# Kernel optimization log

Measured on AMD Instinct MI355X. Metric: run time of the kernel, lower is better.

Reference implementation:

```python
import jax, jax.numpy as jnp
import numpy as np


def setup_inputs() -> dict:
    key = jax.random.key(0)
    k1, k2, k3, k4 = jax.random.split(key, 4)
    B, N, M, D = 8, 2048, 2048, 256
    x = jax.random.normal(k1, (B, N, D), dtype=jnp.float32)
    Fi = jax.random.normal(k2, (B, M, D), dtype=jnp.float32)
    # nn.Linear(dim, dim) params (W applied as x @ W.T + b); scale like torch default
    bound = 1.0 / np.sqrt(D)
    W = jax.random.uniform(k3, (D, D), dtype=jnp.float32, minval=-bound, maxval=bound)
    b = jax.random.uniform(k4, (D,), dtype=jnp.float32, minval=-bound, maxval=bound)
    return {"x": x, "Fi": Fi, "W": W, "b": b}


def reference(x, Fi, W, b):
    # x: [B, N, D], Fi: [B, M, D]
    q = jnp.einsum("bnd,ed->bne", x, W) + b          # linear projection
    scores = jnp.einsum("bnd,bmd->bnm", q, Fi)        # QK^T (no scaling in original)
    attn = jax.nn.softmax(scores, axis=-1)            # softmax over keys
    out = jnp.einsum("bnm,bmd->bnd", attn, Fi)        # attention @ V (V = Fi)
    return out
```

## Files before the change

### kernel.cpp

```cpp
#include <hip/hip_runtime.h>
#include <hip/hip_bf16.h>

typedef _Float16 half8 __attribute__((ext_vector_type(8)));
typedef float floatx4 __attribute__((ext_vector_type(4)));

#define MFMA16H(a, b, c) __builtin_amdgcn_mfma_f32_16x16x32_f16((a), (b), (c), 0, 0, 0)

static constexpr int Bb = 8, Nn = 2048, Mm = 2048, Dd = 256;
static constexpr int FT_ROWS = 272;

__device__ inline void async16(const void* g, void* l)
{
    __builtin_amdgcn_global_load_lds((const __attribute__((address_space(1))) unsigned int*)g,
                                     (__attribute__((address_space(3))) unsigned int*)l,
                                     16, 0, 0);
}

__device__ inline half8 cvt8h(const float* __restrict__ p)
{
    float4 f0 = *reinterpret_cast<const float4*>(p);
    float4 f1 = *reinterpret_cast<const float4*>(p + 4);
    half8 r;
    r[0] = (_Float16)f0.x; r[1] = (_Float16)f0.y; r[2] = (_Float16)f0.z; r[3] = (_Float16)f0.w;
    r[4] = (_Float16)f1.x; r[5] = (_Float16)f1.y; r[6] = (_Float16)f1.z; r[7] = (_Float16)f1.w;
    return r;
}

__device__ inline void cvt8h_split(const float* __restrict__ p, half8& h, half8& l)
{
    float4 f0 = *reinterpret_cast<const float4*>(p);
    float4 f1 = *reinterpret_cast<const float4*>(p + 4);
    float f[8] = {f0.x, f0.y, f0.z, f0.w, f1.x, f1.y, f1.z, f1.w};
#pragma unroll
    for (int i = 0; i < 8; ++i) {
        _Float16 hh = (_Float16)f[i];
        h[i] = hh;
        l[i] = (_Float16)(f[i] - (float)hh);
    }
}

__global__ __launch_bounds__(256, 4)
void prep_kernel(const float* __restrict__ Fi, const float* __restrict__ W,
                 _Float16* __restrict__ FiH, _Float16* __restrict__ FiT,
                 _Float16* __restrict__ Wh, _Float16* __restrict__ Wl)
{
    const int bid = blockIdx.x;
    const int t = threadIdx.x;

    if (bid >= 1056) {
        const int idx = (bid - 1056) * 256 + t;
        const long e = (long)idx * 16;
        const int b  = (int)(e >> 15);
        const int rem = (int)(e & 32767);
        const int rr = rem >> 11;
        const int key = rem & 2047;
        _Float16 v = (rr == 0) ? (_Float16)1.0f : (_Float16)0.0f;
        union { half8 h; uint4 u; } pk;
#pragma unroll
        for (int i = 0; i < 8; ++i) pk.h[i] = v;
        unsigned short* dst = reinterpret_cast<unsigned short*>(FiT)
            + ((size_t)b * FT_ROWS + 256 + rr) * Mm + key;
        *(uint4*)dst       = pk.u;
        *(uint4*)(dst + 8) = pk.u;
        return;
    }
    if (bid >= 1024) {
        const size_t base = (size_t)(bid - 1024) * 2048 + t * 8;
        half8 h, l;
        cvt8h_split(W + base, h, l);
        *(half8*)(Wh + base) = h;
        *(half8*)(Wl + base) = l;
        return;
    }

    __shared__ __align__(16) unsigned short tile[64][72];
    const int b  = bid >> 7;
    const int mt = (bid >> 2) & 31;
    const int dt = bid & 3;
    {
        const int i = t >> 2, jc = (t & 3) * 16;
        const float* src = Fi + ((size_t)b * Mm + mt * 64 + i) * Dd + dt * 64 + jc;
        union { half8 v; uint4 u; } p0, p1;
        p0.v = cvt8h(src);
        p1.v = cvt8h(src + 8);
        *(uint4*)&tile[i][jc]     = p0.u;
        *(uint4*)&tile[i][jc + 8] = p1.u;
        unsigned short* dh = reinterpret_cast<unsigned short*>(FiH)
            + ((size_t)b * Mm + mt * 64 + i) * Dd + dt * 64 + jc;
        *(uint4*)dh       = p0.u;
        *(uint4*)(dh + 8) = p1.u;
    }
    __syncthreads();
    {
        const int d = t >> 2, mc = (t & 3) * 16;
        unsigned short* dst = reinterpret_cast<unsigned short*>(FiT)
            + ((size_t)b * FT_ROWS + dt * 64 + d) * Mm + mt * 64 + mc;
        union { uint4 v[2]; unsigned short s[16]; } u;
#pragma unroll
        for (int s = 0; s < 16; ++s) u.s[s] = tile[mc + s][d];
        *(uint4*)dst       = u.v[0];
        *(uint4*)(dst + 8) = u.v[1];
    }
}

__global__ __launch_bounds__(128, 2)
void qproj_kernel(const float* __restrict__ x, const _Float16* __restrict__ Wh,
                  const _Float16* __restrict__ Wl, const float* __restrict__ bias,
                  _Float16* __restrict__ q)
{
    const int lane = threadIdx.x & 63;
    const int w = threadIdx.x >> 6;
    const int lo = lane & 15, hi = lane >> 4;
    const long r0 = (long)blockIdx.x * 32;

    floatx4 acc[2][8];
#pragma unroll
    for (int rt = 0; rt < 2; ++rt)
#pragma unroll
        for (int j = 0; j < 8; ++j) acc[rt][j] = (floatx4)0.0f;

#pragma unroll
    for (int kk = 0; kk < 8; ++kk) {
        half8 ah[2], al[2];
#pragma unroll
        for (int rt = 0; rt < 2; ++rt)
            cvt8h_split(x + (size_t)(r0 + rt * 16 + lo) * Dd + kk * 32 + hi * 8, ah[rt], al[rt]);
#pragma unroll
        for (int j = 0; j < 8; ++j) {
            const int e = (w * 8 + j) * 16 + lo;
            const size_t wb = (size_t)e * Dd + kk * 32 + hi * 8;
            half8 bh = *reinterpret_cast<const half8*>(Wh + wb);
            half8 bl = *reinterpret_cast<const half8*>(Wl + wb);
#pragma unroll
            for (int rt = 0; rt < 2; ++rt) {
                acc[rt][j] = MFMA16H(ah[rt], bh, acc[rt][j]);
                acc[rt][j] = MFMA16H(ah[rt], bl, acc[rt][j]);
                acc[rt][j] = MFMA16H(al[rt], bh, acc[rt][j]);
            }
        }
    }
#pragma unroll
    for (int j = 0; j < 8; ++j) {
        const int e = (w * 8 + j) * 16 + lo;
        const float bv = bias[e];
#pragma unroll
        for (int rt = 0; rt < 2; ++rt)
#pragma unroll
            for (int r = 0; r < 4; ++r)
                q[(size_t)(r0 + rt * 16 + hi * 4 + r) * Dd + e] = (_Float16)(acc[rt][j][r] + bv);
    }
}

__global__ __launch_bounds__(256, 2)
void flash_kernel(const _Float16* __restrict__ q, const _Float16* __restrict__ FiH,
                  const _Float16* __restrict__ FiT, _Float16* __restrict__ o_part,
                  float* __restrict__ m_part, float* __restrict__ l_part)
{
    __shared__ __align__(16) _Float16 sFi[32 * 256];
    __shared__ __align__(16) _Float16 sFiT[FT_ROWS * 32];
    __shared__ __align__(16) _Float16 sP[4][32 * 40];

    const int bid = blockIdx.x;
    const int b  = bid & 7;
    const int u  = bid >> 3;
    const int nt = u & 15;
    const int kh = u >> 4;
    const int tid = threadIdx.x;
    const int lane = tid & 63, w = tid >> 6;
    const int lo = lane & 15, hi = lane >> 4;
    const int nbase = nt * 128 + w * 32;

    const _Float16* fH = FiH + (size_t)b * Mm * Dd;
    const _Float16* fT = FiT + (size_t)b * FT_ROWS * Mm;

    half8 qf[2][8];
    const _Float16* qb = q + ((size_t)b * Nn + nbase + lo) * Dd + hi * 8;
#pragma unroll
    for (int rt = 0; rt < 2; ++rt)
#pragma unroll
        for (int kk = 0; kk < 8; ++kk)
            qf[rt][kk] = *reinterpret_cast<const half8*>(qb + rt * 16 * Dd + kk * 32);

    floatx4 o[2][16];
    floatx4 ol[2];
#pragma unroll
    for (int rt = 0; rt < 2; ++rt) {
#pragma unroll
        for (int t = 0; t < 16; ++t) o[rt][t] = (floatx4)0.0f;
        ol[rt] = (floatx4)0.0f;
    }
    float m_i[2][4];
#pragma unroll
    for (int rt = 0; rt < 2; ++rt)
#pragma unroll
        for (int r = 0; r < 4; ++r) m_i[rt][r] = -INFINITY;

    for (int it = 0; it < 16; ++it) {
        const int key0 = kh * 512 + it * 32;

        __syncthreads();
#pragma unroll
        for (int j = 0; j < 4; ++j) {
            const int rbase = (w * 4 + j) * 2;
            const int r = rbase + (lane >> 5);
            const int gc = (lane & 31) ^ (r & 7);
            async16(fH + (size_t)(key0 + r) * Dd + gc * 8, &sFi[rbase * 256]);
        }
#pragma unroll
        for (int j = 0; j < 4; ++j) {
            const int rbase = (w + j * 4) * 16;
            const int r = rbase + (lane >> 2);
            const int gc = (lane & 3) ^ (r & 3);
            async16(fT + (size_t)r * Mm + key0 + gc * 8, &sFiT[rbase * 32]);
        }
        if (w == 0) {
            const int r = 256 + (lane >> 2);
            const int gc = (lane & 3) ^ (r & 3);
            async16(fT + (size_t)r * Mm + key0 + gc * 8, &sFiT[256 * 32]);
        }
        __syncthreads();

        floatx4 s[2][2];
#pragma unroll
        for (int rt = 0; rt < 2; ++rt)
#pragma unroll
            for (int st = 0; st < 2; ++st) s[rt][st] = (floatx4)0.0f;
#pragma unroll
        for (int st = 0; st < 2; ++st) {
            const int row = st * 16 + lo;
#pragma unroll
            for (int kk = 0; kk < 8; ++kk) {
                half8 bv = *reinterpret_cast<const half8*>(
                    &sFi[row * 256 + (((kk * 4 + hi) ^ (lo & 7)) * 8)]);
                s[0][st] = MFMA16H(qf[0][kk], bv, s[0][st]);
                s[1][st] = MFMA16H(qf[1][kk], bv, s[1][st]);
            }
        }

        float mn[2][4];
        bool chg = false;
#pragma unroll
        for (int rt = 0; rt < 2; ++rt)
#pragma unroll
            for (int r = 0; r < 4; ++r) {
                float mc = fmaxf(s[rt][0][r], s[rt][1][r]);
                mc = fmaxf(mc, __shfl_xor(mc, 1));
                mc = fmaxf(mc, __shfl_xor(mc, 2));
                mc = fmaxf(mc, __shfl_xor(mc, 4));
                mc = fmaxf(mc, __shfl_xor(mc, 8));
                mn[rt][r] = fmaxf(m_i[rt][r], mc);
                chg = chg || (mn[rt][r] > m_i[rt][r]);
            }
        if (__any(chg)) {
#pragma unroll
            for (int rt = 0; rt < 2; ++rt) {
                float al4[4];
#pragma unroll
                for (int r = 0; r < 4; ++r) {
                    al4[r] = __expf(m_i[rt][r] - mn[rt][r]);
                    m_i[rt][r] = mn[rt][r];
                }
#pragma unroll
                for (int t = 0; t < 16; ++t) {
                    floatx4 ot = o[rt][t];
#pragma unroll
                    for (int r = 0; r < 4; ++r) ot[r] *= al4[r];
                    o[rt][t] = ot;
                }
#pragma unroll
                for (int r = 0; r < 4; ++r) ol[rt][r] *= al4[r];
            }
        }
#pragma unroll
        for (int rt = 0; rt < 2; ++rt)
#pragma unroll
            for (int r = 0; r < 4; ++r) {
                _Float16 p0 = (_Float16)__expf(s[rt][0][r] - m_i[rt][r]);
                _Float16 p1 = (_Float16)__expf(s[rt][1][r] - m_i[rt][r]);
                sP[w][(rt * 16 + hi * 4 + r) * 40 + lo]      = p0;
                sP[w][(rt * 16 + hi * 4 + r) * 40 + 16 + lo] = p1;
            }

        half8 pa0 = *reinterpret_cast<const half8*>(&sP[w][lo * 40 + hi * 8]);
        half8 pa1 = *reinterpret_cast<const half8*>(&sP[w][(16 + lo) * 40 + hi * 8]);
#pragma unroll
        for (int t = 0; t < 16; ++t) {
            half8 bv = *reinterpret_cast<const half8*>(
                &sFiT[(t * 16 + lo) * 32 + ((hi ^ (lo & 3)) * 8)]);
            o[0][t] = MFMA16H(pa0, bv, o[0][t]);
            o[1][t] = MFMA16H(pa1, bv, o[1][t]);
        }
        {
            half8 bvl = *reinterpret_cast<const half8*>(
                &sFiT[(256 + lo) * 32 + ((hi ^ (lo & 3)) * 8)]);
            ol[0] = MFMA16H(pa0, bvl, ol[0]);
            ol[1] = MFMA16H(pa1, bvl, ol[1]);
        }
    }

#pragma unroll
    for (int rt = 0; rt < 2; ++rt)
#pragma unroll
        for (int r = 0; r < 4; ++r) {
            const long gq = (long)b * Nn + nbase + rt * 16 + hi * 4 + r;
            const size_t obase = ((size_t)kh * (Bb * Nn) + gq) * Dd;
#pragma unroll
            for (int t = 0; t < 16; ++t)
                o_part[obase + t * 16 + lo] = (_Float16)o[rt][t][r];
            if (lo == 0) {
                m_part[(size_t)kh * (Bb * Nn) + gq] = m_i[rt][r];
                l_part[(size_t)kh * (Bb * Nn) + gq] = ol[rt][r];
            }
        }
}

__global__ __launch_bounds__(256, 8)
void merge_kernel(const _Float16* __restrict__ o_part, const float* __restrict__ m_part,
                  const float* __restrict__ l_part, float* __restrict__ out)
{
    const int row = blockIdx.x;
    const int col = threadIdx.x;
    float m[4], l[4];
#pragma unroll
    for (int k = 0; k < 4; ++k) {
        m[k] = m_part[(size_t)k * (Bb * Nn) + row];
        l[k] = l_part[(size_t)k * (Bb * Nn) + row];
    }
    float M = fmaxf(fmaxf(m[0], m[1]), fmaxf(m[2], m[3]));
    float denom = 0.f, acc = 0.f;
#pragma unroll
    for (int k = 0; k < 4; ++k) {
        const float wk = __expf(m[k] - M);
        denom += wk * l[k];
        acc += wk * (float)o_part[((size_t)k * (Bb * Nn) + row) * Dd + col];
    }
    out[(size_t)row * Dd + col] = acc / denom;
}

extern "C" void kernel_launch(void* const* d_in, const int* in_sizes, int n_in,
                              void* d_out, int out_size, void* d_ws, size_t ws_size,
                              hipStream_t stream)
{
    const float* x    = (const float*)d_in[0];
    const float* Fi   = (const float*)d_in[1];
    const float* W    = (const float*)d_in[2];
    const float* bias = (const float*)d_in[3];
    float* out = (float*)d_out;

    _Float16* q_ws = (_Float16*)d_ws;
    _Float16* FiH  = q_ws + (size_t)Bb * Nn * Dd;
    _Float16* FiT  = FiH + (size_t)Bb * Mm * Dd;
    _Float16* Wh   = FiT + (size_t)Bb * FT_ROWS * Mm;
    _Float16* Wl   = Wh + (size_t)Dd * Dd;
    _Float16* o_part = Wl + (size_t)Dd * Dd;
    float* m_part  = (float*)(o_part + (size_t)4 * Bb * Nn * Dd);
    float* l_part  = m_part + (size_t)4 * Bb * Nn;

    hipLaunchKernelGGL(prep_kernel, dim3(1120), dim3(256), 0, stream, Fi, W, FiH, FiT, Wh, Wl);
    hipLaunchKernelGGL(qproj_kernel, dim3(512), dim3(128), 0, stream, x, Wh, Wl, bias, q_ws);
    hipLaunchKernelGGL(flash_kernel, dim3(512), dim3(256), 0, stream, q_ws, FiH, FiT,
                       o_part, m_part, l_part);
    hipLaunchKernelGGL(merge_kernel, dim3(16384), dim3(256), 0, stream, o_part, m_part, l_part, out);
}
```

Before: 247.0 us.

## Double-buffer key tiles in flash kernel and compute row sums with a ones fragment

The flash kernel now double-buffers the Fi and FiT shared-memory tiles, so async loads of the next key tile overlap with the MFMA work on the current one. The extra ones/zeros rows that were appended to FiT for the row-sum are replaced by an in-register ones vector, which removes a fill pass in prep and one LDS read per step. The sP padding drops from 40 to 36, and qproj switches to 16-row blocks with higher occupancy. The cost is roughly double the LDS per block, which may limit how many blocks fit per CU, and the smaller sP pad may change bank conflicts.

```diff
diff --git a/kernel.cpp b/kernel.cpp
--- a/kernel.cpp
+++ b/kernel.cpp
@@ -7,7 +7,6 @@
 #define MFMA16H(a, b, c) __builtin_amdgcn_mfma_f32_16x16x32_f16((a), (b), (c), 0, 0, 0)
 
 static constexpr int Bb = 8, Nn = 2048, Mm = 2048, Dd = 256;
-static constexpr int FT_ROWS = 272;
 
 __device__ inline void async16(const void* g, void* l)
 {
@@ -47,23 +46,6 @@
     const int bid = blockIdx.x;
     const int t = threadIdx.x;
 
-    if (bid >= 1056) {
-        const int idx = (bid - 1056) * 256 + t;
-        const long e = (long)idx * 16;
-        const int b  = (int)(e >> 15);
-        const int rem = (int)(e & 32767);
-        const int rr = rem >> 11;
-        const int key = rem & 2047;
-        _Float16 v = (rr == 0) ? (_Float16)1.0f : (_Float16)0.0f;
-        union { half8 h; uint4 u; } pk;
-#pragma unroll
-        for (int i = 0; i < 8; ++i) pk.h[i] = v;
-        unsigned short* dst = reinterpret_cast<unsigned short*>(FiT)
-            + ((size_t)b * FT_ROWS + 256 + rr) * Mm + key;
-        *(uint4*)dst       = pk.u;
-        *(uint4*)(dst + 8) = pk.u;
-        return;
-    }
     if (bid >= 1024) {
         const size_t base = (size_t)(bid - 1024) * 2048 + t * 8;
         half8 h, l;
@@ -94,7 +76,7 @@
     {
         const int d = t >> 2, mc = (t & 3) * 16;
         unsigned short* dst = reinterpret_cast<unsigned short*>(FiT)
-            + ((size_t)b * FT_ROWS + dt * 64 + d) * Mm + mt * 64 + mc;
+            + ((size_t)b * Dd + dt * 64 + d) * Mm + mt * 64 + mc;
         union { uint4 v[2]; unsigned short s[16]; } u;
 #pragma unroll
         for (int s = 0; s < 16; ++s) u.s[s] = tile[mc + s][d];
@@ -103,7 +85,7 @@
     }
 }
 
-__global__ __launch_bounds__(128, 2)
+__global__ __launch_bounds__(128, 4)
 void qproj_kernel(const float* __restrict__ x, const _Float16* __restrict__ Wh,
                   const _Float16* __restrict__ Wl, const float* __restrict__ bias,
                   _Float16* __restrict__ q)
@@ -111,32 +93,25 @@
     const int lane = threadIdx.x & 63;
     const int w = threadIdx.x >> 6;
     const int lo = lane & 15, hi = lane >> 4;
-    const long r0 = (long)blockIdx.x * 32;
-
-    floatx4 acc[2][8];
-#pragma unroll
-    for (int rt = 0; rt < 2; ++rt)
-#pragma unroll
-        for (int j = 0; j < 8; ++j) acc[rt][j] = (floatx4)0.0f;
+    const long r0 = (long)blockIdx.x * 16;
+
+    floatx4 acc[8];
+#pragma unroll
+    for (int j = 0; j < 8; ++j) acc[j] = (floatx4)0.0f;
 
 #pragma unroll
     for (int kk = 0; kk < 8; ++kk) {
-        half8 ah[2], al[2];
-#pragma unroll
-        for (int rt = 0; rt < 2; ++rt)
-            cvt8h_split(x + (size_t)(r0 + rt * 16 + lo) * Dd + kk * 32 + hi * 8, ah[rt], al[rt]);
+        half8 ah, al;
+        cvt8h_split(x + (size_t)(r0 + lo) * Dd + kk * 32 + hi * 8, ah, al);
 #pragma unroll
         for (int j = 0; j < 8; ++j) {
             const int e = (w * 8 + j) * 16 + lo;
             const size_t wb = (size_t)e * Dd + kk * 32 + hi * 8;
             half8 bh = *reinterpret_cast<const half8*>(Wh + wb);
             half8 bl = *reinterpret_cast<const half8*>(Wl + wb);
-#pragma unroll
-            for (int rt = 0; rt < 2; ++rt) {
-                acc[rt][j] = MFMA16H(ah[rt], bh, acc[rt][j]);
-                acc[rt][j] = MFMA16H(ah[rt], bl, acc[rt][j]);
-                acc[rt][j] = MFMA16H(al[rt], bh, acc[rt][j]);
-            }
+            acc[j] = MFMA16H(ah, bh, acc[j]);
+            acc[j] = MFMA16H(ah, bl, acc[j]);
+            acc[j] = MFMA16H(al, bh, acc[j]);
         }
     }
 #pragma unroll
@@ -144,10 +119,8 @@
         const int e = (w * 8 + j) * 16 + lo;
         const float bv = bias[e];
 #pragma unroll
-        for (int rt = 0; rt < 2; ++rt)
-#pragma unroll
-            for (int r = 0; r < 4; ++r)
-                q[(size_t)(r0 + rt * 16 + hi * 4 + r) * Dd + e] = (_Float16)(acc[rt][j][r] + bv);
+        for (int r = 0; r < 4; ++r)
+            q[(size_t)(r0 + hi * 4 + r) * Dd + e] = (_Float16)(acc[j][r] + bv);
     }
 }
 
@@ -156,9 +129,11 @@
                   const _Float16* __restrict__ FiT, _Float16* __restrict__ o_part,
                   float* __restrict__ m_part, float* __restrict__ l_part)
 {
-    __shared__ __align__(16) _Float16 sFi[32 * 256];
-    __shared__ __align__(16) _Float16 sFiT[FT_ROWS * 32];
-    __shared__ __align__(16) _Float16 sP[4][32 * 40];
+    __shared__ __align__(16) _Float16 sFiA[32 * 256];
+    __shared__ __align__(16) _Float16 sFiB[32 * 256];
+    __shared__ __align__(16) _Float16 sFiTA[256 * 32];
+    __shared__ __align__(16) _Float16 sFiTB[256 * 32];
+    __shared__ __align__(16) _Float16 sP[4][32 * 36];
 
     const int bid = blockIdx.x;
     const int b  = bid & 7;
@@ -171,7 +146,7 @@
     const int nbase = nt * 128 + w * 32;
 
     const _Float16* fH = FiH + (size_t)b * Mm * Dd;
-    const _Float16* fT = FiT + (size_t)b * FT_ROWS * Mm;
+    const _Float16* fT = FiT + (size_t)b * Dd * Mm;
 
     half8 qf[2][8];
     const _Float16* qb = q + ((size_t)b * Nn + nbase + lo) * Dd + hi * 8;
@@ -181,6 +156,10 @@
         for (int kk = 0; kk < 8; ++kk)
             qf[rt][kk] = *reinterpret_cast<const half8*>(qb + rt * 16 * Dd + kk * 32);
 
+    half8 ones;
+#pragma unroll
+    for (int i = 0; i < 8; ++i) ones[i] = (_Float16)1.0f;
+
     floatx4 o[2][16];
     floatx4 ol[2];
 #pragma unroll
@@ -195,31 +174,25 @@
 #pragma unroll
         for (int r = 0; r < 4; ++r) m_i[rt][r] = -INFINITY;
 
-    for (int it = 0; it < 16; ++it) {
+    auto stage = [&](int it, _Float16* dFi, _Float16* dFiT) {
         const int key0 = kh * 512 + it * 32;
-
-        __syncthreads();
 #pragma unroll
         for (int j = 0; j < 4; ++j) {
             const int rbase = (w * 4 + j) * 2;
             const int r = rbase + (lane >> 5);
             const int gc = (lane & 31) ^ (r & 7);
-            async16(fH + (size_t)(key0 + r) * Dd + gc * 8, &sFi[rbase * 256]);
+            async16(fH + (size_t)(key0 + r) * Dd + gc * 8, dFi + rbase * 256);
         }
 #pragma unroll
         for (int j = 0; j < 4; ++j) {
             const int rbase = (w + j * 4) * 16;
             const int r = rbase + (lane >> 2);
             const int gc = (lane & 3) ^ (r & 3);
-            async16(fT + (size_t)r * Mm + key0 + gc * 8, &sFiT[rbase * 32]);
-        }
-        if (w == 0) {
-            const int r = 256 + (lane >> 2);
-            const int gc = (lane & 3) ^ (r & 3);
-            async16(fT + (size_t)r * Mm + key0 + gc * 8, &sFiT[256 * 32]);
-        }
-        __syncthreads();
-
+            async16(fT + (size_t)r * Mm + key0 + gc * 8, dFiT + rbase * 32);
+        }
+    };
+
+    auto compute = [&](const _Float16* SFI, const _Float16* SFIT) {
         floatx4 s[2][2];
 #pragma unroll
         for (int rt = 0; rt < 2; ++rt)
@@ -231,7 +204,7 @@
 #pragma unroll
             for (int kk = 0; kk < 8; ++kk) {
                 half8 bv = *reinterpret_cast<const half8*>(
-                    &sFi[row * 256 + (((kk * 4 + hi) ^ (lo & 7)) * 8)]);
+                    SFI + row * 256 + (((kk * 4 + hi) ^ (lo & 7)) * 8));
                 s[0][st] = MFMA16H(qf[0][kk], bv, s[0][st]);
                 s[1][st] = MFMA16H(qf[1][kk], bv, s[1][st]);
             }
@@ -277,25 +250,31 @@
             for (int r = 0; r < 4; ++r) {
                 _Float16 p0 = (_Float16)__expf(s[rt][0][r] - m_i[rt][r]);
                 _Float16 p1 = (_Float16)__expf(s[rt][1][r] - m_i[rt][r]);
-                sP[w][(rt * 16 + hi * 4 + r) * 40 + lo]      = p0;
-                sP[w][(rt * 16 + hi * 4 + r) * 40 + 16 + lo] = p1;
-            }
-
-        half8 pa0 = *reinterpret_cast<const half8*>(&sP[w][lo * 40 + hi * 8]);
-        half8 pa1 = *reinterpret_cast<const half8*>(&sP[w][(16 + lo) * 40 + hi * 8]);
+                sP[w][(rt * 16 + hi * 4 + r) * 36 + lo]      = p0;
+                sP[w][(rt * 16 + hi * 4 + r) * 36 + 16 + lo] = p1;
+            }
+
+        half8 pa0 = *reinterpret_cast<const half8*>(&sP[w][lo * 36 + hi * 8]);
+        half8 pa1 = *reinterpret_cast<const half8*>(&sP[w][(16 + lo) * 36 + hi * 8]);
 #pragma unroll
         for (int t = 0; t < 16; ++t) {
             half8 bv = *reinterpret_cast<const half8*>(
-                &sFiT[(t * 16 + lo) * 32 + ((hi ^ (lo & 3)) * 8)]);
+                SFIT + (t * 16 + lo) * 32 + ((hi ^ (lo & 3)) * 8));
             o[0][t] = MFMA16H(pa0, bv, o[0][t]);
             o[1][t] = MFMA16H(pa1, bv, o[1][t]);
         }
-        {
-            half8 bvl = *reinterpret_cast<const half8*>(
-                &sFiT[(256 + lo) * 32 + ((hi ^ (lo & 3)) * 8)]);
-            ol[0] = MFMA16H(pa0, bvl, ol[0]);
-            ol[1] = MFMA16H(pa1, bvl, ol[1]);
-        }
+        ol[0] = MFMA16H(pa0, ones, ol[0]);
+        ol[1] = MFMA16H(pa1, ones, ol[1]);
+    };
+
+    stage(0, sFiA, sFiTA);
+    for (int it = 0; it < 16; it += 2) {
+        __syncthreads();
+        stage(it + 1, sFiB, sFiTB);
+        compute(sFiA, sFiTA);
+        __syncthreads();
+        if (it + 2 < 16) stage(it + 2, sFiA, sFiTA);
+        compute(sFiB, sFiTB);
     }
 
 #pragma unroll
@@ -350,14 +329,14 @@
     _Float16* q_ws = (_Float16*)d_ws;
     _Float16* FiH  = q_ws + (size_t)Bb * Nn * Dd;
     _Float16* FiT  = FiH + (size_t)Bb * Mm * Dd;
-    _Float16* Wh   = FiT + (size_t)Bb * FT_ROWS * Mm;
+    _Float16* Wh   = FiT + (size_t)Bb * Dd * Mm;
     _Float16* Wl   = Wh + (size_t)Dd * Dd;
     _Float16* o_part = Wl + (size_t)Dd * Dd;
     float* m_part  = (float*)(o_part + (size_t)4 * Bb * Nn * Dd);
     float* l_part  = m_part + (size_t)4 * Bb * Nn;
 
-    hipLaunchKernelGGL(prep_kernel, dim3(1120), dim3(256), 0, stream, Fi, W, FiH, FiT, Wh, Wl);
-    hipLaunchKernelGGL(qproj_kernel, dim3(512), dim3(128), 0, stream, x, Wh, Wl, bias, q_ws);
+    hipLaunchKernelGGL(prep_kernel, dim3(1056), dim3(256), 0, stream, Fi, W, FiH, FiT, Wh, Wl);
+    hipLaunchKernelGGL(qproj_kernel, dim3(1024), dim3(128), 0, stream, x, Wh, Wl, bias, q_ws);
     hipLaunchKernelGGL(flash_kernel, dim3(512), dim3(256), 0, stream, q_ws, FiH, FiT,
                        o_part, m_part, l_part);
     hipLaunchKernelGGL(merge_kernel, dim3(16384), dim3(256), 0, stream, o_part, m_part, l_part, out);
```

Result: faster. 231.9 us (-6.1%).
